# Optimization experiments

Measured on AMD Instinct MI355X. Metric: run time of the kernel, lower is better.

## Reference

```python
import jax, jax.numpy as jnp
import numpy as np

H = 128          # hidden_channels
N_USER = 100000
N_ITEM = 50000
E = 1000000      # number of labeled edges


def setup_inputs() -> dict:
    key = jax.random.key(0)
    ks = jax.random.split(key, 6)
    z_user = jax.random.normal(ks[0], (N_USER, H), dtype=jnp.float32)
    z_item = jax.random.normal(ks[1], (N_ITEM, H), dtype=jnp.float32)
    row = jax.random.randint(ks[2], (E,), 0, N_USER, dtype=jnp.int64 if jax.config.jax_enable_x64 else jnp.int32)
    col = jax.random.randint(ks[3], (E,), 0, N_ITEM, dtype=jnp.int64 if jax.config.jax_enable_x64 else jnp.int32)
    W1 = jax.random.normal(ks[4], (2 * H, H), dtype=jnp.float32) / np.sqrt(2 * H)
    b1 = jnp.zeros((H,), dtype=jnp.float32)
    W2 = jax.random.normal(ks[5], (H, 1), dtype=jnp.float32) / np.sqrt(H)
    b2 = jnp.zeros((1,), dtype=jnp.float32)
    return {"z_user": z_user, "z_item": z_item, "row": row, "col": col,
            "W1": W1, "b1": b1, "W2": W2, "b2": b2}


def reference(z_user, z_item, row, col, W1, b1, W2, b2):
    # z = cat([z_user[row], z_item[col]], -1); lin1(z).relu(); lin2 -> view(-1)
    # Split W1 so we never materialize the [E, 2H] concat explicitly as one buffer:
    # cat([a, b]) @ W1 == a @ W1[:H] + b @ W1[H:]
    W1u, W1i = W1[:H], W1[H:]
    h = z_user[row] @ W1u + z_item[col] @ W1i + b1          # [E, H]
    h = jax.nn.relu(h)
    out = h @ W2 + b2                                        # [E, 1]
    return out.reshape(-1)
```

## Files before the change

### kernel.cpp

```cpp
#include <hip/hip_runtime.h>

#define HH 128
#define BU 8
#define BI 32
#define NBKT (BU * BI)
#define SCHUNK 4096

typedef __attribute__((ext_vector_type(8))) short bf16x8;
typedef __attribute__((ext_vector_type(4))) float f32x4;
typedef unsigned long long u64;

__device__ inline unsigned short f2bf(float f) {
    unsigned u = __builtin_bit_cast(unsigned, f);
    u += 0x7FFF + ((u >> 16) & 1);
    return (unsigned short)(u >> 16);
}

__device__ inline int bucket_of(int u, int i, unsigned n_user, unsigned n_item) {
    unsigned uc = ((unsigned)u * BU) / n_user;
    unsigned ic = ((unsigned)i * BI) / n_item;
    return (int)(uc * BI + ic);
}

__global__ __launch_bounds__(256) void project_both_kernel(
    const float* __restrict__ Zu, const float* __restrict__ Zi,
    const float* __restrict__ W1, const float* __restrict__ b1,
    unsigned short* __restrict__ Pu, unsigned short* __restrict__ Pi,
    int n_user, int n_item, int ublocks)
{
    __shared__ unsigned short sWt[128 * 128];
    __shared__ unsigned short sOut[64 * 136];

    const bool isUser = ((int)blockIdx.x < ublocks);
    const float* __restrict__ Z = isUser ? Zu : Zi;
    const float* __restrict__ W = isUser ? W1 : (W1 + HH * HH);
    unsigned short* __restrict__ P = isUser ? Pu : Pi;
    const int nrows  = isUser ? n_user : n_item;
    const int ntiles = (nrows + 63) >> 6;
    const int tbase  = (isUser ? (int)blockIdx.x : ((int)blockIdx.x - ublocks)) * 2;

    const int t    = threadIdx.x;
    const int wave = t >> 6;
    const int lane = t & 63;
    const int l16  = lane & 15;
    const int lk8  = (lane >> 4) * 8;

    #pragma unroll 4
    for (int i = 0; i < 16; ++i) {
        int idx = t + i * 256;
        int k   = idx >> 5;
        int c4  = (idx & 31) * 4;
        float4 w = *(const float4*)(W + (size_t)k * HH + c4);
        float wv[4] = {w.x, w.y, w.z, w.w};
        #pragma unroll
        for (int j = 0; j < 4; ++j) {
            int c = c4 + j;
            sWt[c * 128 + (((k >> 3) ^ (c & 15)) << 3) + (k & 7)] = f2bf(wv[j]);
        }
    }

    float b1r[8];
    #pragma unroll
    for (int nt = 0; nt < 8; ++nt)
        b1r[nt] = isUser ? b1[nt * 16 + l16] : 0.f;

    __syncthreads();

    #pragma unroll 1
    for (int s = 0; s < 2; ++s) {
        const int tile = tbase + s;
        if (tile >= ntiles) break;
        const int rbase = tile << 6;

        f32x4 acc[8];
        #pragma unroll
        for (int nt = 0; nt < 8; ++nt) acc[nt] = (f32x4)0.f;

        int m = rbase + wave * 16 + l16;
        if (m > nrows - 1) m = nrows - 1;
        const float* Zrow = Z + (size_t)m * HH;

        #pragma unroll
        for (int kk = 0; kk < 4; ++kk) {
            float4 z0 = *(const float4*)(Zrow + kk * 32 + lk8);
            float4 z1 = *(const float4*)(Zrow + kk * 32 + lk8 + 4);
            bf16x8 a;
            a[0] = (short)f2bf(z0.x); a[1] = (short)f2bf(z0.y);
            a[2] = (short)f2bf(z0.z); a[3] = (short)f2bf(z0.w);
            a[4] = (short)f2bf(z1.x); a[5] = (short)f2bf(z1.y);
            a[6] = (short)f2bf(z1.z); a[7] = (short)f2bf(z1.w);

            const int chunkSw = ((kk * 4 + (lane >> 4)) ^ l16) << 3;
            #pragma unroll
            for (int nt = 0; nt < 8; ++nt) {
                int c = nt * 16 + l16;
                bf16x8 b = *(const bf16x8*)(sWt + c * 128 + chunkSw);
                acc[nt] = __builtin_amdgcn_mfma_f32_16x16x32_bf16(a, b, acc[nt], 0, 0, 0);
            }
        }

        __syncthreads();
        #pragma unroll
        for (int nt = 0; nt < 8; ++nt) {
            int colc = nt * 16 + l16;
            #pragma unroll
            for (int r = 0; r < 4; ++r) {
                int orow = wave * 16 + (lane >> 4) * 4 + r;
                sOut[orow * 136 + colc] = f2bf(acc[nt][r] + b1r[nt]);
            }
        }
        __syncthreads();
        #pragma unroll
        for (int i = 0; i < 4; ++i) {
            int idx = t + i * 256;
            int r   = idx >> 4;
            int ch  = idx & 15;
            int grow = rbase + r;
            if (grow < nrows)
                *(uint4*)(P + (size_t)grow * HH + ch * 8) =
                    *(const uint4*)(sOut + r * 136 + ch * 8);
        }
    }
}

__global__ __launch_bounds__(256) void init_cursor_kernel(unsigned* __restrict__ cursor, int cap)
{
    cursor[threadIdx.x] = (unsigned)(threadIdx.x * cap);
}

__global__ __launch_bounds__(256) void scatter_kernel(
    const int* __restrict__ row, const int* __restrict__ col,
    unsigned* __restrict__ cursor, u64* __restrict__ srt,
    unsigned* __restrict__ invpos, int E, unsigned n_user, unsigned n_item)
{
    __shared__ unsigned lh[NBKT];
    __shared__ unsigned gb[NBKT];
    __shared__ unsigned lc[NBKT];
    const int t    = threadIdx.x;
    const int base = blockIdx.x * SCHUNK;

    int uu[SCHUNK / 256], ii[SCHUNK / 256], bk[SCHUNK / 256];

    lh[t] = 0;
    __syncthreads();
    #pragma unroll
    for (int k = 0; k < SCHUNK / 256; ++k) {
        int e = base + k * 256 + t;
        bk[k] = -1;
        if (e < E) {
            uu[k] = row[e]; ii[k] = col[e];
            bk[k] = bucket_of(uu[k], ii[k], n_user, n_item);
            atomicAdd(&lh[bk[k]], 1u);
        }
    }
    __syncthreads();
    gb[t] = lh[t] ? atomicAdd(&cursor[t], lh[t]) : 0u;
    lc[t] = 0;
    __syncthreads();
    #pragma unroll
    for (int k = 0; k < SCHUNK / 256; ++k) {
        int e = base + k * 256 + t;
        if (e < E) {
            int b = bk[k];
            unsigned r   = atomicAdd(&lc[b], 1u);
            unsigned pos = gb[b] + r;
            srt[pos]  = ((u64)(unsigned)uu[k] << 32) | (u64)(unsigned)ii[k];
            invpos[e] = pos;
        }
    }
}

__global__ __launch_bounds__(256) void edge_sorted_kernel(
    const unsigned short* __restrict__ Pu, const unsigned short* __restrict__ Pi,
    const u64* __restrict__ srt, const unsigned* __restrict__ cursor,
    const float* __restrict__ W2, const float* __restrict__ b2,
    float* __restrict__ psorted, int cap)
{
    const int uc     = blockIdx.x & (BU - 1);
    const int jj     = blockIdx.x >> 3;
    const int g      = threadIdx.x >> 4;
    const int lane16 = threadIdx.x & 15;
    const int gg     = jj * 16 + g;
    const int c0     = lane16 * 8;

    float w2r[8];
    #pragma unroll
    for (int q = 0; q < 8; ++q) w2r[q] = W2[c0 + q];
    const float b2s = b2[0];

    #pragma unroll 1
    for (int ic = 0; ic < BI; ++ic) {
        const int b    = uc * BI + ic;
        const int S    = b * cap;
        const int Tend = (int)cursor[b];
        for (int p = S + gg; p < Tend; p += BU * 512) {
            u64 pk = srt[p];
            int u  = (int)(pk >> 32);
            int it = (int)(pk & 0xFFFFFFFFu);
            uint4 pu = *(const uint4*)(Pu + (size_t)u  * HH + c0);
            uint4 pi = *(const uint4*)(Pi + (size_t)it * HH + c0);
            unsigned a[4] = {pu.x, pu.y, pu.z, pu.w};
            unsigned c[4] = {pi.x, pi.y, pi.z, pi.w};
            float pv = 0.f;
            #pragma unroll
            for (int q = 0; q < 4; ++q) {
                float x0 = __builtin_bit_cast(float, a[q] << 16);
                float x1 = __builtin_bit_cast(float, a[q] & 0xFFFF0000u);
                float y0 = __builtin_bit_cast(float, c[q] << 16);
                float y1 = __builtin_bit_cast(float, c[q] & 0xFFFF0000u);
                pv = fmaf(fmaxf(x0 + y0, 0.f), w2r[2 * q],     pv);
                pv = fmaf(fmaxf(x1 + y1, 0.f), w2r[2 * q + 1], pv);
            }
            #pragma unroll
            for (int m = 8; m >= 1; m >>= 1)
                pv += __shfl_xor(pv, m, 64);
            if (lane16 == 0) psorted[p] = pv + b2s;
        }
    }
}

__global__ __launch_bounds__(256) void permute_kernel(
    const float* __restrict__ psorted, const unsigned* __restrict__ invpos,
    float* __restrict__ out, int E)
{
    int i  = blockIdx.x * blockDim.x + threadIdx.x;
    int st = gridDim.x * blockDim.x;
    for (int e = i; e < E; e += st)
        out[e] = psorted[invpos[e]];
}

__global__ __launch_bounds__(256) void edge_bf16_kernel(
    const unsigned short* __restrict__ Pu, const unsigned short* __restrict__ Pi,
    const int* __restrict__ row, const int* __restrict__ col,
    const float* __restrict__ W2, const float* __restrict__ b2,
    float* __restrict__ out, int E)
{
    const int lane16 = threadIdx.x & 15;
    const int gid    = (blockIdx.x * blockDim.x + threadIdx.x) >> 4;
    const int stride = (gridDim.x * blockDim.x) >> 4;
    const int c0     = lane16 * 8;

    float w2r[8];
    #pragma unroll
    for (int q = 0; q < 8; ++q) w2r[q] = W2[c0 + q];
    const float b2s = b2[0];

    for (int e = gid; e < E; e += stride) {
        int u = row[e], it = col[e];
        uint4 pu = *(const uint4*)(Pu + (size_t)u  * HH + c0);
        uint4 pi = *(const uint4*)(Pi + (size_t)it * HH + c0);
        unsigned a[4] = {pu.x, pu.y, pu.z, pu.w};
        unsigned b[4] = {pi.x, pi.y, pi.z, pi.w};
        float p = 0.f;
        #pragma unroll
        for (int q = 0; q < 4; ++q) {
            float x0 = __builtin_bit_cast(float, a[q] << 16);
            float x1 = __builtin_bit_cast(float, a[q] & 0xFFFF0000u);
            float y0 = __builtin_bit_cast(float, b[q] << 16);
            float y1 = __builtin_bit_cast(float, b[q] & 0xFFFF0000u);
            p = fmaf(fmaxf(x0 + y0, 0.f), w2r[2 * q],     p);
            p = fmaf(fmaxf(x1 + y1, 0.f), w2r[2 * q + 1], p);
        }
        #pragma unroll
        for (int m = 8; m >= 1; m >>= 1)
            p += __shfl_xor(p, m, 64);
        if (lane16 == 0) out[e] = p + b2s;
    }
}

__global__ __launch_bounds__(256) void edge_direct_kernel(
    const float* __restrict__ zu, const float* __restrict__ zi,
    const int* __restrict__ row, const int* __restrict__ col,
    const float* __restrict__ W1, const float* __restrict__ b1,
    const float* __restrict__ W2, const float* __restrict__ b2,
    float* __restrict__ out, int E)
{
    const int lane   = threadIdx.x & 31;
    const int gid    = (blockIdx.x * blockDim.x + threadIdx.x) >> 5;
    const int stride = (gridDim.x * blockDim.x) >> 5;
    const int c0     = lane * 4;

    const float4 b1v = *(const float4*)(b1 + c0);
    const float4 w2v = *(const float4*)(W2 + c0);
    const float  b2s = b2[0];

    for (int e = gid; e < E; e += stride) {
        int u  = row[e];
        int it = col[e];
        const float* zur = zu + (size_t)u  * HH;
        const float* zir = zi + (size_t)it * HH;
        float4 acc = b1v;
        for (int k = 0; k < HH; ++k) {
            float  zk = zur[k];
            float4 w  = *(const float4*)(W1 + (size_t)k * HH + c0);
            acc.x = fmaf(zk, w.x, acc.x);
            acc.y = fmaf(zk, w.y, acc.y);
            acc.z = fmaf(zk, w.z, acc.z);
            acc.w = fmaf(zk, w.w, acc.w);
        }
        for (int k = 0; k < HH; ++k) {
            float  zk = zir[k];
            float4 w  = *(const float4*)(W1 + (size_t)(HH + k) * HH + c0);
            acc.x = fmaf(zk, w.x, acc.x);
            acc.y = fmaf(zk, w.y, acc.y);
            acc.z = fmaf(zk, w.z, acc.z);
            acc.w = fmaf(zk, w.w, acc.w);
        }
        float p = fmaxf(acc.x, 0.f) * w2v.x;
        p = fmaf(fmaxf(acc.y, 0.f), w2v.y, p);
        p = fmaf(fmaxf(acc.z, 0.f), w2v.z, p);
        p = fmaf(fmaxf(acc.w, 0.f), w2v.w, p);
        #pragma unroll
        for (int m = 16; m >= 1; m >>= 1)
            p += __shfl_xor(p, m, 64);
        if (lane == 0) out[e] = p + b2s;
    }
}

static inline size_t align256(size_t x) { return (x + 255) & ~(size_t)255; }

extern "C" void kernel_launch(void* const* d_in, const int* in_sizes, int n_in,
                              void* d_out, int out_size, void* d_ws, size_t ws_size,
                              hipStream_t stream)
{
    const float* z_user = (const float*)d_in[0];
    const float* z_item = (const float*)d_in[1];
    const int*   row    = (const int*)d_in[2];
    const int*   col    = (const int*)d_in[3];
    const float* W1     = (const float*)d_in[4];
    const float* b1     = (const float*)d_in[5];
    const float* W2     = (const float*)d_in[6];
    const float* b2     = (const float*)d_in[7];
    float*       out    = (float*)d_out;

    const int n_user = in_sizes[0] / HH;
    const int n_item = in_sizes[1] / HH;
    const int E      = in_sizes[2];

    const int capBase = (E + NBKT - 1) / NBKT;
    const int cap     = capBase + capBase / 4 + 64;
    const size_t padded = (size_t)cap * NBKT;

    const size_t offPu  = 0;
    const size_t offPi  = align256(offPu  + (size_t)n_user * HH * 2);
    const size_t offSrt = align256(offPi  + (size_t)n_item * HH * 2);
    const size_t offPs  = align256(offSrt + padded * 8);
    const size_t offInv = align256(offPs  + padded * 4);
    const size_t offCur = align256(offInv + (size_t)E * 4);
    const size_t needSort = align256(offCur + NBKT * 4);
    const size_t needProj = align256(offPi + (size_t)n_item * HH * 2);

    const bool sortable = (n_user >= BU) && (n_item >= BI) &&
                          (n_user <= (1 << 17)) && (ws_size >= needSort);

    const int utiles  = (n_user + 63) >> 6;
    const int itiles  = (n_item + 63) >> 6;
    const int ublocks = (utiles + 1) >> 1;
    const int iblocks = (itiles + 1) >> 1;

    if (sortable) {
        unsigned short* Pu  = (unsigned short*)((char*)d_ws + offPu);
        unsigned short* Pi  = (unsigned short*)((char*)d_ws + offPi);
        u64*            srt = (u64*)((char*)d_ws + offSrt);
        float*          ps  = (float*)((char*)d_ws + offPs);
        unsigned*       inv = (unsigned*)((char*)d_ws + offInv);
        unsigned*       cur = (unsigned*)((char*)d_ws + offCur);

        init_cursor_kernel<<<1, NBKT, 0, stream>>>(cur, cap);
        scatter_kernel<<<(E + SCHUNK - 1) / SCHUNK, 256, 0, stream>>>(
            row, col, cur, srt, inv, E, (unsigned)n_user, (unsigned)n_item);
        project_both_kernel<<<ublocks + iblocks, 256, 0, stream>>>(
            z_user, z_item, W1, b1, Pu, Pi, n_user, n_item, ublocks);
        edge_sorted_kernel<<<2048, 256, 0, stream>>>(Pu, Pi, srt, cur, W2, b2, ps, cap);
        permute_kernel<<<1024, 256, 0, stream>>>(ps, inv, out, E);
    } else if (ws_size >= needProj) {
        unsigned short* Pu = (unsigned short*)((char*)d_ws + offPu);
        unsigned short* Pi = (unsigned short*)((char*)d_ws + offPi);
        project_both_kernel<<<ublocks + iblocks, 256, 0, stream>>>(
            z_user, z_item, W1, b1, Pu, Pi, n_user, n_item, ublocks);
        edge_bf16_kernel<<<2048, 256, 0, stream>>>(Pu, Pi, row, col, W2, b2, out, E);
    } else {
        edge_direct_kernel<<<2048, 256, 0, stream>>>(z_user, z_item, row, col, W1, b1, W2, b2, out, E);
    }
}
```

Baseline: 113.5 us.

## Fuse scatter with projection, pack sort keys to 32 bits, use fp16 dot2 edge math

```diff
diff --git a/kernel.cpp b/kernel.cpp
--- a/kernel.cpp
+++ b/kernel.cpp
@@ -4,42 +4,91 @@
 #define BU 8
 #define BI 32
 #define NBKT (BU * BI)
-#define SCHUNK 4096
+#define SCHUNK 2048
 
 typedef __attribute__((ext_vector_type(8))) short bf16x8;
 typedef __attribute__((ext_vector_type(4))) float f32x4;
+typedef _Float16 h2 __attribute__((ext_vector_type(2)));
 typedef unsigned long long u64;
+
+#if __has_builtin(__builtin_amdgcn_fdot2)
+#define FDOT2(a, b, c) __builtin_amdgcn_fdot2((a), (b), (c), false)
+#else
+#define FDOT2(a, b, c) ((c) + (float)(a)[0] * (float)(b)[0] + (float)(a)[1] * (float)(b)[1])
+#endif
 
 __device__ inline unsigned short f2bf(float f) {
     unsigned u = __builtin_bit_cast(unsigned, f);
     u += 0x7FFF + ((u >> 16) & 1);
     return (unsigned short)(u >> 16);
 }
-
-__device__ inline int bucket_of(int u, int i, unsigned n_user, unsigned n_item) {
-    unsigned uc = ((unsigned)u * BU) / n_user;
-    unsigned ic = ((unsigned)i * BI) / n_item;
-    return (int)(uc * BI + ic);
-}
-
-__global__ __launch_bounds__(256) void project_both_kernel(
+__device__ inline unsigned short f2h(float f) {
+    return __builtin_bit_cast(unsigned short, (_Float16)f);
+}
+
+__global__ __launch_bounds__(256) void mega_kernel(
     const float* __restrict__ Zu, const float* __restrict__ Zi,
     const float* __restrict__ W1, const float* __restrict__ b1,
     unsigned short* __restrict__ Pu, unsigned short* __restrict__ Pi,
-    int n_user, int n_item, int ublocks)
+    const int* __restrict__ row, const int* __restrict__ col,
+    unsigned* __restrict__ cursor, unsigned* __restrict__ srt,
+    unsigned* __restrict__ invpos,
+    int n_user, int n_item, int E, int cap, int scatBlocks, int ublocks)
 {
     __shared__ unsigned short sWt[128 * 128];
     __shared__ unsigned short sOut[64 * 136];
 
-    const bool isUser = ((int)blockIdx.x < ublocks);
+    const int t = threadIdx.x;
+
+    if ((int)blockIdx.x < scatBlocks) {
+        unsigned* lh = (unsigned*)sWt;
+        unsigned* gb = lh + NBKT;
+        unsigned* lc = gb + NBKT;
+        const int base = blockIdx.x * SCHUNK;
+
+        int uu[SCHUNK / 256], ii[SCHUNK / 256];
+        lh[t] = 0;
+        __syncthreads();
+        #pragma unroll
+        for (int k = 0; k < SCHUNK / 256; ++k) {
+            int e = base + k * 256 + t;
+            if (e < E) {
+                uu[k] = row[e]; ii[k] = col[e];
+                unsigned uc = ((unsigned)uu[k] * BU) / (unsigned)n_user;
+                unsigned ic = ((unsigned)ii[k] * BI) / (unsigned)n_item;
+                atomicAdd(&lh[uc * BI + ic], 1u);
+            }
+        }
+        __syncthreads();
+        gb[t] = lh[t] ? (unsigned)(t * cap) + atomicAdd(&cursor[t], lh[t]) : 0u;
+        lc[t] = 0;
+        __syncthreads();
+        #pragma unroll
+        for (int k = 0; k < SCHUNK / 256; ++k) {
+            int e = base + k * 256 + t;
+            if (e < E) {
+                unsigned uc = ((unsigned)uu[k] * BU) / (unsigned)n_user;
+                unsigned ic = ((unsigned)ii[k] * BI) / (unsigned)n_item;
+                int b = (int)(uc * BI + ic);
+                unsigned ucbase = (uc * (unsigned)n_user + 7u) >> 3;
+                unsigned r   = atomicAdd(&lc[b], 1u);
+                unsigned pos = gb[b] + r;
+                srt[pos]  = (((unsigned)uu[k] - ucbase) << 16) | (unsigned)ii[k];
+                invpos[e] = pos;
+            }
+        }
+        return;
+    }
+
+    const int pbid = (int)blockIdx.x - scatBlocks;
+    const bool isUser = (pbid < ublocks);
     const float* __restrict__ Z = isUser ? Zu : Zi;
     const float* __restrict__ W = isUser ? W1 : (W1 + HH * HH);
     unsigned short* __restrict__ P = isUser ? Pu : Pi;
     const int nrows  = isUser ? n_user : n_item;
     const int ntiles = (nrows + 63) >> 6;
-    const int tbase  = (isUser ? (int)blockIdx.x : ((int)blockIdx.x - ublocks)) * 2;
-
-    const int t    = threadIdx.x;
+    const int tbase  = (isUser ? pbid : (pbid - ublocks)) * 2;
+
     const int wave = t >> 6;
     const int lane = t & 63;
     const int l16  = lane & 15;
@@ -106,7 +155,7 @@
             #pragma unroll
             for (int r = 0; r < 4; ++r) {
                 int orow = wave * 16 + (lane >> 4) * 4 + r;
-                sOut[orow * 136 + colc] = f2bf(acc[nt][r] + b1r[nt]);
+                sOut[orow * 136 + colc] = f2h(acc[nt][r] + b1r[nt]);
             }
         }
         __syncthreads();
@@ -123,98 +172,57 @@
     }
 }
 
-__global__ __launch_bounds__(256) void init_cursor_kernel(unsigned* __restrict__ cursor, int cap)
-{
-    cursor[threadIdx.x] = (unsigned)(threadIdx.x * cap);
-}
-
-__global__ __launch_bounds__(256) void scatter_kernel(
-    const int* __restrict__ row, const int* __restrict__ col,
-    unsigned* __restrict__ cursor, u64* __restrict__ srt,
-    unsigned* __restrict__ invpos, int E, unsigned n_user, unsigned n_item)
-{
-    __shared__ unsigned lh[NBKT];
-    __shared__ unsigned gb[NBKT];
-    __shared__ unsigned lc[NBKT];
-    const int t    = threadIdx.x;
-    const int base = blockIdx.x * SCHUNK;
-
-    int uu[SCHUNK / 256], ii[SCHUNK / 256], bk[SCHUNK / 256];
-
-    lh[t] = 0;
-    __syncthreads();
-    #pragma unroll
-    for (int k = 0; k < SCHUNK / 256; ++k) {
-        int e = base + k * 256 + t;
-        bk[k] = -1;
-        if (e < E) {
-            uu[k] = row[e]; ii[k] = col[e];
-            bk[k] = bucket_of(uu[k], ii[k], n_user, n_item);
-            atomicAdd(&lh[bk[k]], 1u);
-        }
-    }
-    __syncthreads();
-    gb[t] = lh[t] ? atomicAdd(&cursor[t], lh[t]) : 0u;
-    lc[t] = 0;
-    __syncthreads();
-    #pragma unroll
-    for (int k = 0; k < SCHUNK / 256; ++k) {
-        int e = base + k * 256 + t;
-        if (e < E) {
-            int b = bk[k];
-            unsigned r   = atomicAdd(&lc[b], 1u);
-            unsigned pos = gb[b] + r;
-            srt[pos]  = ((u64)(unsigned)uu[k] << 32) | (u64)(unsigned)ii[k];
-            invpos[e] = pos;
-        }
-    }
-}
-
 __global__ __launch_bounds__(256) void edge_sorted_kernel(
     const unsigned short* __restrict__ Pu, const unsigned short* __restrict__ Pi,
-    const u64* __restrict__ srt, const unsigned* __restrict__ cursor,
+    const unsigned* __restrict__ srt, const unsigned* __restrict__ cursor,
     const float* __restrict__ W2, const float* __restrict__ b2,
-    float* __restrict__ psorted, int cap)
+    float* __restrict__ psorted, int cap, int n_user)
 {
     const int uc     = blockIdx.x & (BU - 1);
     const int jj     = blockIdx.x >> 3;
-    const int g      = threadIdx.x >> 4;
-    const int lane16 = threadIdx.x & 15;
-    const int gg     = jj * 16 + g;
-    const int c0     = lane16 * 8;
-
-    float w2r[8];
+    const int g      = threadIdx.x >> 3;
+    const int lane8  = threadIdx.x & 7;
+    const int gg     = jj * 32 + g;
+    const int c0     = lane8 * 16;
+    const int ucbase = (int)(((unsigned)uc * (unsigned)n_user + 7u) >> 3);
+
+    h2 w2h[8];
     #pragma unroll
-    for (int q = 0; q < 8; ++q) w2r[q] = W2[c0 + q];
+    for (int j = 0; j < 8; ++j) {
+        w2h[j][0] = (_Float16)W2[c0 + 2 * j];
+        w2h[j][1] = (_Float16)W2[c0 + 2 * j + 1];
+    }
     const float b2s = b2[0];
+    const h2 hz = {(_Float16)0, (_Float16)0};
 
     #pragma unroll 1
     for (int ic = 0; ic < BI; ++ic) {
         const int b    = uc * BI + ic;
         const int S    = b * cap;
-        const int Tend = (int)cursor[b];
-        for (int p = S + gg; p < Tend; p += BU * 512) {
-            u64 pk = srt[p];
-            int u  = (int)(pk >> 32);
-            int it = (int)(pk & 0xFFFFFFFFu);
-            uint4 pu = *(const uint4*)(Pu + (size_t)u  * HH + c0);
-            uint4 pi = *(const uint4*)(Pi + (size_t)it * HH + c0);
-            unsigned a[4] = {pu.x, pu.y, pu.z, pu.w};
-            unsigned c[4] = {pi.x, pi.y, pi.z, pi.w};
-            float pv = 0.f;
+        const int Tend = S + (int)cursor[b];
+        for (int p = S + gg; p < Tend; p += BU * 1024) {
+            unsigned pk = srt[p];
+            int u  = ucbase + (int)(pk >> 16);
+            int it = (int)(pk & 0xFFFFu);
+            const unsigned short* pur = Pu + (size_t)u  * HH + c0;
+            const unsigned short* pir = Pi + (size_t)it * HH + c0;
+            uint4 a0 = *(const uint4*)pur;
+            uint4 a1 = *(const uint4*)(pur + 8);
+            uint4 c0v = *(const uint4*)pir;
+            uint4 c1v = *(const uint4*)(pir + 8);
+            unsigned aw[8] = {a0.x, a0.y, a0.z, a0.w, a1.x, a1.y, a1.z, a1.w};
+            unsigned cw[8] = {c0v.x, c0v.y, c0v.z, c0v.w, c1v.x, c1v.y, c1v.z, c1v.w};
+            float acc = 0.f;
             #pragma unroll
-            for (int q = 0; q < 4; ++q) {
-                float x0 = __builtin_bit_cast(float, a[q] << 16);
-                float x1 = __builtin_bit_cast(float, a[q] & 0xFFFF0000u);
-                float y0 = __builtin_bit_cast(float, c[q] << 16);
-                float y1 = __builtin_bit_cast(float, c[q] & 0xFFFF0000u);
-                pv = fmaf(fmaxf(x0 + y0, 0.f), w2r[2 * q],     pv);
-                pv = fmaf(fmaxf(x1 + y1, 0.f), w2r[2 * q + 1], pv);
+            for (int q = 0; q < 8; ++q) {
+                h2 s = __builtin_bit_cast(h2, aw[q]) + __builtin_bit_cast(h2, cw[q]);
+                s = __builtin_elementwise_max(s, hz);
+                acc = FDOT2(s, w2h[q], acc);
             }
-            #pragma unroll
-            for (int m = 8; m >= 1; m >>= 1)
-                pv += __shfl_xor(pv, m, 64);
-            if (lane16 == 0) psorted[p] = pv + b2s;
+            acc += __shfl_xor(acc, 4, 64);
+            acc += __shfl_xor(acc, 2, 64);
+            acc += __shfl_xor(acc, 1, 64);
+            if (lane8 == 0) psorted[p] = acc + b2s;
         }
     }
 }
@@ -229,42 +237,47 @@
         out[e] = psorted[invpos[e]];
 }
 
-__global__ __launch_bounds__(256) void edge_bf16_kernel(
+__global__ __launch_bounds__(256) void edge_fp16_kernel(
     const unsigned short* __restrict__ Pu, const unsigned short* __restrict__ Pi,
     const int* __restrict__ row, const int* __restrict__ col,
     const float* __restrict__ W2, const float* __restrict__ b2,
     float* __restrict__ out, int E)
 {
-    const int lane16 = threadIdx.x & 15;
-    const int gid    = (blockIdx.x * blockDim.x + threadIdx.x) >> 4;
-    const int stride = (gridDim.x * blockDim.x) >> 4;
-    const int c0     = lane16 * 8;
-
-    float w2r[8];
+    const int lane8  = threadIdx.x & 7;
+    const int gid    = (blockIdx.x * blockDim.x + threadIdx.x) >> 3;
+    const int stride = (gridDim.x * blockDim.x) >> 3;
+    const int c0     = lane8 * 16;
+
+    h2 w2h[8];
     #pragma unroll
-    for (int q = 0; q < 8; ++q) w2r[q] = W2[c0 + q];
+    for (int j = 0; j < 8; ++j) {
+        w2h[j][0] = (_Float16)W2[c0 + 2 * j];
+        w2h[j][1] = (_Float16)W2[c0 + 2 * j + 1];
+    }
     const float b2s = b2[0];
+    const h2 hz = {(_Float16)0, (_Float16)0};
 
     for (int e = gid; e < E; e += stride) {
         int u = row[e], it = col[e];
-        uint4 pu = *(const uint4*)(Pu + (size_t)u  * HH + c0);
-        uint4 pi = *(const uint4*)(Pi + (size_t)it * HH + c0);
-        unsigned a[4] = {pu.x, pu.y, pu.z, pu.w};
-        unsigned b[4] = {pi.x, pi.y, pi.z, pi.w};
-        float p = 0.f;
-        #pragma unroll
-        for (int q = 0; q < 4; ++q) {
-            float x0 = __builtin_bit_cast(float, a[q] << 16);
-            float x1 = __builtin_bit_cast(float, a[q] & 0xFFFF0000u);
-            float y0 = __builtin_bit_cast(float, b[q] << 16);
-            float y1 = __builtin_bit_cast(float, b[q] & 0xFFFF0000u);
-            p = fmaf(fmaxf(x0 + y0, 0.f), w2r[2 * q],     p);
-            p = fmaf(fmaxf(x1 + y1, 0.f), w2r[2 * q + 1], p);
-        }
-        #pragma unroll
-        for (int m = 8; m >= 1; m >>= 1)
-            p += __shfl_xor(p, m, 64);
-        if (lane16 == 0) out[e] = p + b2s;
+        const unsigned short* pur = Pu + (size_t)u  * HH + c0;
+        const unsigned short* pir = Pi + (size_t)it * HH + c0;
+        uint4 a0 = *(const uint4*)pur;
+        uint4 a1 = *(const uint4*)(pur + 8);
+        uint4 c0v = *(const uint4*)pir;
+        uint4 c1v = *(const uint4*)(pir + 8);
+        unsigned aw[8] = {a0.x, a0.y, a0.z, a0.w, a1.x, a1.y, a1.z, a1.w};
+        unsigned cw[8] = {c0v.x, c0v.y, c0v.z, c0v.w, c1v.x, c1v.y, c1v.z, c1v.w};
+        float acc = 0.f;
+        #pragma unroll
+        for (int q = 0; q < 8; ++q) {
+            h2 s = __builtin_bit_cast(h2, aw[q]) + __builtin_bit_cast(h2, cw[q]);
+            s = __builtin_elementwise_max(s, hz);
+            acc = FDOT2(s, w2h[q], acc);
+        }
+        acc += __shfl_xor(acc, 4, 64);
+        acc += __shfl_xor(acc, 2, 64);
+        acc += __shfl_xor(acc, 1, 64);
+        if (lane8 == 0) out[e] = acc + b2s;
     }
 }
 
@@ -344,41 +357,44 @@
     const size_t offPu  = 0;
     const size_t offPi  = align256(offPu  + (size_t)n_user * HH * 2);
     const size_t offSrt = align256(offPi  + (size_t)n_item * HH * 2);
-    const size_t offPs  = align256(offSrt + padded * 8);
+    const size_t offPs  = align256(offSrt + padded * 4);
     const size_t offInv = align256(offPs  + padded * 4);
     const size_t offCur = align256(offInv + (size_t)E * 4);
     const size_t needSort = align256(offCur + NBKT * 4);
     const size_t needProj = align256(offPi + (size_t)n_item * HH * 2);
 
     const bool sortable = (n_user >= BU) && (n_item >= BI) &&
+                          (n_item < 65536) && (n_user / BU + 1 < 65536) &&
                           (n_user <= (1 << 17)) && (ws_size >= needSort);
 
     const int utiles  = (n_user + 63) >> 6;
     const int itiles  = (n_item + 63) >> 6;
     const int ublocks = (utiles + 1) >> 1;
     const int iblocks = (itiles + 1) >> 1;
+    const int scatBlocks = (E + SCHUNK - 1) / SCHUNK;
 
     if (sortable) {
         unsigned short* Pu  = (unsigned short*)((char*)d_ws + offPu);
         unsigned short* Pi  = (unsigned short*)((char*)d_ws + offPi);
-        u64*            srt = (u64*)((char*)d_ws + offSrt);
+        unsigned*       srt = (unsigned*)((char*)d_ws + offSrt);
         float*          ps  = (float*)((char*)d_ws + offPs);
         unsigned*       inv = (unsigned*)((char*)d_ws + offInv);
         unsigned*       cur = (unsigned*)((char*)d_ws + offCur);
 
-        init_cursor_kernel<<<1, NBKT, 0, stream>>>(cur, cap);
-        scatter_kernel<<<(E + SCHUNK - 1) / SCHUNK, 256, 0, stream>>>(
-            row, col, cur, srt, inv, E, (unsigned)n_user, (unsigned)n_item);
-        project_both_kernel<<<ublocks + iblocks, 256, 0, stream>>>(
-            z_user, z_item, W1, b1, Pu, Pi, n_user, n_item, ublocks);
-        edge_sorted_kernel<<<2048, 256, 0, stream>>>(Pu, Pi, srt, cur, W2, b2, ps, cap);
+        hipMemsetAsync(cur, 0, NBKT * 4, stream);
+        mega_kernel<<<scatBlocks + ublocks + iblocks, 256, 0, stream>>>(
+            z_user, z_item, W1, b1, Pu, Pi, row, col, cur, srt, inv,
+            n_user, n_item, E, cap, scatBlocks, ublocks);
+        edge_sorted_kernel<<<2048, 256, 0, stream>>>(Pu, Pi, srt, cur, W2, b2, ps, cap, n_user);
         permute_kernel<<<1024, 256, 0, stream>>>(ps, inv, out, E);
     } else if (ws_size >= needProj) {
         unsigned short* Pu = (unsigned short*)((char*)d_ws + offPu);
         unsigned short* Pi = (unsigned short*)((char*)d_ws + offPi);
-        project_both_kernel<<<ublocks + iblocks, 256, 0, stream>>>(
-            z_user, z_item, W1, b1, Pu, Pi, n_user, n_item, ublocks);
-        edge_bf16_kernel<<<2048, 256, 0, stream>>>(Pu, Pi, row, col, W2, b2, out, E);
+        mega_kernel<<<ublocks + iblocks, 256, 0, stream>>>(
+            z_user, z_item, W1, b1, Pu, Pi, row, col,
+            (unsigned*)nullptr, (unsigned*)nullptr, (unsigned*)nullptr,
+            n_user, n_item, E, cap, 0, ublocks);
+        edge_fp16_kernel<<<2048, 256, 0, stream>>>(Pu, Pi, row, col, W2, b2, out, E);
     } else {
         edge_direct_kernel<<<2048, 256, 0, stream>>>(z_user, z_item, row, col, W1, b1, W2, b2, out, E);
     }
```

Measured after the change: 101.1 us. 10.8% less time.
